# Kernel optimization log

Hardware: AMD Instinct MI355X
Metric: run time of the kernel (lower is better)

## Reference

```python
import jax, jax.numpy as jnp
import numpy as np

VX, VY = 0.16, 0.16
X0, Y0 = 0.0, -39.68
BN_EPS = 1e-5
P, M, C_IN, C_OUT = 40000, 100, 9, 64


def setup_inputs() -> dict:
    key = jax.random.key(0)
    ks = jax.random.split(key, 8)
    return {
        "pillar_x": jax.random.normal(ks[0], (P, M), dtype=jnp.float32),
        "pillar_y": jax.random.normal(ks[1], (P, M), dtype=jnp.float32),
        "pillar_z": jax.random.normal(ks[2], (P, M), dtype=jnp.float32),
        "pillar_i": jax.random.uniform(ks[3], (P, M), dtype=jnp.float32),
        "num_points_per_pillar": jax.random.randint(ks[4], (P,), 0, M, dtype=jnp.int32),
        "coors": jax.random.randint(ks[5], (P, 4), 0, 496, dtype=jnp.int32),
        "W": jax.random.normal(ks[6], (C_IN, C_OUT), dtype=jnp.float32) * 0.1,
        "gamma": jnp.ones((C_OUT,), dtype=jnp.float32),
        "beta": jnp.zeros((C_OUT,), dtype=jnp.float32),
    }


def reference(pillar_x, pillar_y, pillar_z, pillar_i, num_points_per_pillar, coors, W, gamma, beta):
    dtype = pillar_x.dtype
    max_points = pillar_x.shape[1]
    # per-pillar point count, clamped to >=1 (matches torch.clamp(min=1))
    n = jnp.clip(num_points_per_pillar, 1, None).astype(dtype)[:, None]  # (P,1)
    mean_x = jnp.sum(pillar_x, axis=1, keepdims=True) / n
    mean_y = jnp.sum(pillar_y, axis=1, keepdims=True) / n
    mean_z = jnp.sum(pillar_z, axis=1, keepdims=True) / n
    x_off = pillar_x - mean_x
    y_off = pillar_y - mean_y
    z_off = pillar_z - mean_z
    # BEV pillar-center coordinates, broadcast over points
    x_bev = (coors[:, 3].astype(dtype) * VX + VX / 2 + X0)[:, None] * jnp.ones((1, max_points), dtype)
    y_bev = (coors[:, 2].astype(dtype) * VY + VY / 2 + Y0)[:, None] * jnp.ones((1, max_points), dtype)
    # validity mask: point index < num_points (vectorized version of the python loop)
    mask = (jnp.arange(max_points)[None, :] < num_points_per_pillar[:, None]).astype(dtype)
    feats = jnp.stack(
        [pillar_x, pillar_y, pillar_z, pillar_i, x_off, y_off, z_off, x_bev, y_bev],
        axis=-1,
    )  # (P, M, 9)
    feats = feats * mask[:, :, None]
    # PFNLayer: Linear (no bias) -> BatchNorm1d (training-mode batch stats) -> ReLU -> max over points
    x = jnp.einsum("pmc,cd->pmd", feats, W)  # (P, M, 64)
    mu = jnp.mean(x, axis=(0, 1))
    var = jnp.var(x, axis=(0, 1))  # biased variance, as BatchNorm uses
    x = (x - mu) * jax.lax.rsqrt(var + BN_EPS) * gamma + beta
    x = jax.nn.relu(x)
    return jnp.max(x, axis=1)  # (P, 64)
```

## Files before the change

### kernel.cpp

```cpp
#include <hip/hip_runtime.h>

#define P_N 40000
#define M_N 100
#define NBF 10000
#define NPART 80
#define NUSED 74
#define NBUCKET 32

typedef _Float16 half2_t __attribute__((ext_vector_type(2)));

__device__ __forceinline__ float bcf(int x) { return __int_as_float(x); }
__device__ __forceinline__ int   bci(float x) { return __float_as_int(x); }
__device__ __forceinline__ float rlf(float v, int l) {
  return bcf(__builtin_amdgcn_readlane(bci(v), l));
}
__device__ __forceinline__ int pk16i(float a, float b) {
  return __builtin_bit_cast(int, __builtin_amdgcn_cvt_pkrtz(a, b));
}
__device__ __forceinline__ half2_t h2(int x) { return __builtin_bit_cast(half2_t, x); }
__device__ __forceinline__ float dot2(int a, int b, float acc) {
  return __builtin_amdgcn_fdot2(h2(a), h2(b), acc, false);
}

__device__ __forceinline__ float dpp_sum64(float x) {
  x += bcf(__builtin_amdgcn_update_dpp(0, bci(x), 0x111, 0xf, 0xf, true));
  x += bcf(__builtin_amdgcn_update_dpp(0, bci(x), 0x112, 0xf, 0xf, true));
  x += bcf(__builtin_amdgcn_update_dpp(0, bci(x), 0x114, 0xf, 0xf, true));
  x += bcf(__builtin_amdgcn_update_dpp(0, bci(x), 0x118, 0xf, 0xf, true));
  x += bcf(__builtin_amdgcn_update_dpp(0, bci(x), 0x142, 0xf, 0xf, true));
  x += bcf(__builtin_amdgcn_update_dpp(0, bci(x), 0x143, 0xf, 0xf, true));
  return x;
}

__device__ __forceinline__ half2_t uPK(int4 q, half2_t AA, half2_t BB,
                                       half2_t CC, half2_t DD, half2_t EE) {
  half2_t t = h2(q.w) * DD + EE;
  t = h2(q.z) * CC + t;
  t = h2(q.y) * BB + t;
  t = h2(q.x) * AA + t;
  return t;
}


__global__ __launch_bounds__(256) void k_zero(float* __restrict__ buckets) {
  const int i = threadIdx.x;
  #pragma unroll
  for (int k = 0; k < NBUCKET * NPART / 256; ++k) buckets[k * 256 + i] = 0.f;
}


__global__ __launch_bounds__(128) void k_fused(
    const float* __restrict__ px, const float* __restrict__ py,
    const float* __restrict__ pz, const float* __restrict__ pi,
    const int* __restrict__ npp, const int* __restrict__ coors,
    const float* __restrict__ W,
    float* __restrict__ buckets, float* __restrict__ umm)
{
  const int lane = threadIdx.x & 63;
  const int wid  = threadIdx.x >> 6;
  const int d    = lane;

  __shared__ int4  stage[2][2][64];
  __shared__ float red[2][NPART];

  int c = 9, c2 = 9;
  if (lane < 45) {
    int k = lane; c = 0;
    while (k >= 9 - c) { k -= 9 - c; ++c; }
    c2 = c + k;
  } else if (lane < 54) {
    c = lane - 45; c2 = 9;
  }
  const int rc1 = (c  < 4) ? c  : (c  < 7) ? c  - 4 : (c  < 9) ? c  - 2 : 4;
  const int rc2 = (c2 < 4) ? c2 : (c2 < 7) ? c2 - 4 : (c2 < 9) ? c2 - 2 : 4;
  const bool bothVec = (rc1 < 4) && (rc2 < 4);
  const bool statln  = lane < 54;

  float w[9];
  #pragma unroll
  for (int q = 0; q < 9; ++q) w[q] = W[q * 64 + d];
  const float sA = w[0] + w[4], sB = w[1] + w[5], sC = w[2] + w[6], sD = w[3];
  const half2_t AA = h2(pk16i(sA, sA));
  const half2_t BB = h2(pk16i(sB, sB));
  const half2_t CC = h2(pk16i(sC, sC));
  const half2_t DD = h2(pk16i(sD, sD));
  const int H1 = 0x3C003C00;

  const bool act = lane < 50;
  const int wgid  = blockIdx.x * 2 + wid;
  const int pbase = __builtin_amdgcn_readfirstlane(wgid * 2);

  const int2 n2 = ((const int2*)npp)[wgid];
  int4 cc[2];
  cc[0] = ((const int4*)coors)[pbase + 0];
  cc[1] = ((const int4*)coors)[pbase + 1];

  int u0[2], u1[2], u2[2], u3[2];
  #pragma unroll
  for (int it = 0; it < 2; ++it) {
    const int p_ = pbase + it;
    float2 X = make_float2(0.f, 0.f), Y = X, Z = X, I = X;
    if (act) {
      X = ((const float2*)(px + (size_t)p_ * M_N))[lane];
      Y = ((const float2*)(py + (size_t)p_ * M_N))[lane];
      Z = ((const float2*)(pz + (size_t)p_ * M_N))[lane];
      I = ((const float2*)(pi + (size_t)p_ * M_N))[lane];
    }
    u0[it] = pk16i(X.x, X.y);
    u1[it] = pk16i(Y.x, Y.y);
    u2[it] = pk16i(Z.x, Z.y);
    u3[it] = pk16i(I.x, I.y);
    stage[wid][it][lane] = make_int4(u0[it], u1[it], u2[it], u3[it]);
  }

  float R2a[10] = {};
  float corrAcc = 0.f;

  #pragma unroll
  for (int it = 0; it < 2; ++it) {
    const int p_ = pbase + it;
    const int n  = ((const int*)&n2)[it];
    const float nf = (float)n;

    const unsigned msk = ((2 * lane     < n) ? 0x0000FFFFu : 0u)
                       | ((2 * lane + 1 < n) ? 0xFFFF0000u : 0u);
    const int g0 = u0[it] & msk;
    const int g1 = u1[it] & msk;
    const int g2 = u2[it] & msk;
    const int g3 = u3[it] & msk;

    float fx = dot2(u0[it], H1, 0.f);
    float fy = dot2(u1[it], H1, 0.f);
    float fz = dot2(u2[it], H1, 0.f);
    float vx = dot2(g0, H1, 0.f);
    float vy = dot2(g1, H1, 0.f);
    float vz = dot2(g2, H1, 0.f);
    float vi = dot2(g3, H1, 0.f);
    fx = dpp_sum64(fx); fy = dpp_sum64(fy); fz = dpp_sum64(fz);
    vx = dpp_sum64(vx); vy = dpp_sum64(vy); vz = dpp_sum64(vz); vi = dpp_sum64(vi);

    const int nc = n < 1 ? 1 : n;
    const float inv = __builtin_amdgcn_rcpf((float)nc);
    const float mx = rlf(fx, 63) * inv;
    const float my = rlf(fy, 63) * inv;
    const float mz = rlf(fz, 63) * inv;
    const float svx = rlf(vx, 63);
    const float svy = rlf(vy, 63);
    const float svz = rlf(vz, 63);
    const float svi = rlf(vi, 63);

    const float xb = fmaf((float)cc[it].w, 0.16f, 0.08f);
    const float yb = fmaf((float)cc[it].z, 0.16f, 0.08f - 39.68f);

    R2a[0] = dot2(g0, g0, R2a[0]);
    R2a[1] = dot2(g0, g1, R2a[1]);
    R2a[2] = dot2(g0, g2, R2a[2]);
    R2a[3] = dot2(g0, g3, R2a[3]);
    R2a[4] = dot2(g1, g1, R2a[4]);
    R2a[5] = dot2(g1, g2, R2a[5]);
    R2a[6] = dot2(g1, g3, R2a[6]);
    R2a[7] = dot2(g2, g2, R2a[7]);
    R2a[8] = dot2(g2, g3, R2a[8]);
    R2a[9] = dot2(g3, g3, R2a[9]);

    {
      const float nxb = nf * xb, nyb = nf * yb;
      const float S1 = (rc1 == 0) ? svx : (rc1 == 1) ? svy : (rc1 == 2) ? svz
                     : (rc1 == 3) ? svi : (rc1 == 4) ? nf  : (rc1 == 5) ? nxb : nyb;
      const float S2 = (rc2 == 0) ? svx : (rc2 == 1) ? svy : (rc2 == 2) ? svz
                     : (rc2 == 3) ? svi : (rc2 == 4) ? nf  : (rc2 == 5) ? nxb : nyb;
      float base = 0.f;
      if (!bothVec)
        base = (rc1 > 3) ? ((rc1 == 4) ? S2 : (rc1 == 5) ? xb * S2 : yb * S2)
                         : ((rc2 == 4) ? S1 : (rc2 == 5) ? xb * S1 : yb * S1);
      const float mv1 = (c  == 4) ? mx : (c  == 5) ? my : (c  == 6) ? mz : 0.f;
      const float mv2 = (c2 == 4) ? mx : (c2 == 5) ? my : (c2 == 6) ? mz : 0.f;
      const float term = base - mv1 * S2 - mv2 * S1 + nf * mv1 * mv2;
      if (statln) corrAcc += term;
    }

    const float sE = fmaf(-mx, w[4], fmaf(-my, w[5], fmaf(-mz, w[6],
                     fmaf(xb, w[7], yb * w[8]))));
    const half2_t EE = h2(pk16i(sE, sE));

    const int4* sp = &stage[wid][it][0];
    half2_t ap0 = h2((int)0xFC00FC00);
    half2_t ap1 = ap0;
    const int nh = n >> 1;
    int l = 0;
    for (; l + 2 <= nh; l += 2) {
      const int4 qa = sp[l];
      const int4 qb = sp[l + 1];
      ap0 = __builtin_elementwise_max(ap0, uPK(qa, AA, BB, CC, DD, EE));
      ap1 = __builtin_elementwise_max(ap1, uPK(qb, AA, BB, CC, DD, EE));
    }
    if (l < nh)
      ap0 = __builtin_elementwise_max(ap0, uPK(sp[l], AA, BB, CC, DD, EE));
    const half2_t am = __builtin_elementwise_max(ap0, ap1);
    float um = fmaxf((float)am.x, (float)am.y);
    if (n & 1) {
      const int4 qt = sp[nh];
      const float tx = (float)h2(qt.x).x;
      const float ty = (float)h2(qt.y).x;
      const float tz = (float)h2(qt.z).x;
      const float ti = (float)h2(qt.w).x;
      um = fmaxf(um, fmaf(tx, sA, fmaf(ty, sB, fmaf(tz, sC, fmaf(ti, sD, sE)))));
    }
    umm[(size_t)p_ * 64 + d] = um;
  }

  #pragma unroll
  for (int i = 0; i < 10; ++i) R2a[i] = dpp_sum64(R2a[i]);

  red[wid][lane] = corrAcc;
  if (lane == 63) {
    #pragma unroll
    for (int i = 0; i < 10; ++i) red[wid][64 + i] = R2a[i];
  }
  __syncthreads();
  if (threadIdx.x < NUSED) {
    const int t = threadIdx.x;
    atomicAdd(&buckets[(blockIdx.x & (NBUCKET - 1)) * NPART + t],
              red[0][t] + red[1][t]);
  }
}


__global__ __launch_bounds__(64) void k_stats(
    const float* __restrict__ buckets, const float* __restrict__ W,
    const float* __restrict__ gamma, const float* __restrict__ beta,
    float* __restrict__ scale, float* __restrict__ shift)
{
  const int d = threadIdx.x;
  __shared__ float Cs[NUSED];
  {
    float s0 = 0.f, s1 = 0.f;
    #pragma unroll
    for (int b = 0; b < NBUCKET; ++b) {
      s0 += buckets[b * NPART + d];
      if (d < NUSED - 64) s1 += buckets[b * NPART + 64 + d];
    }
    Cs[d] = s0;
    if (d < NUSED - 64) Cs[64 + d] = s1;
  }
  __syncthreads();

  float mom1[9];
  #pragma unroll
  for (int q = 0; q < 9; ++q) mom1[q] = Cs[45 + q];
  float mom2[45];
  {
    int k = 0;
    #pragma unroll
    for (int cA = 0; cA < 9; ++cA) {
      #pragma unroll
      for (int cB = cA; cB < 9; ++cB) {
        float v = Cs[k];
        if (cA <= 6 && cB <= 6) {
          const int a = (cA < 4) ? cA : cA - 4;
          const int b = (cB < 4) ? cB : cB - 4;
          const int lo = a < b ? a : b;
          const int hi = a < b ? b : a;
          const int idx = lo * 4 - lo * (lo - 1) / 2 + (hi - lo);
          v += Cs[64 + idx];
        }
        mom2[k] = v;
        ++k;
      }
    }
  }

  float w[9];
  #pragma unroll
  for (int q = 0; q < 9; ++q) w[q] = W[q * 64 + d];
  const float invN = 1.f / ((float)P_N * (float)M_N);
  float mu = 0.f;
  #pragma unroll
  for (int q = 0; q < 9; ++q) mu += mom1[q] * w[q];
  mu *= invN;
  float e2 = 0.f;
  int k = 0;
  #pragma unroll
  for (int cA = 0; cA < 9; ++cA) {
    #pragma unroll
    for (int cB = cA; cB < 9; ++cB) {
      const float t = w[cA] * w[cB] * mom2[k];
      e2 += (cA == cB) ? t : 2.f * t;
      ++k;
    }
  }
  e2 *= invN;
  float var = e2 - mu * mu;
  var = var < 0.f ? 0.f : var;
  const float sc = gamma[d] * rsqrtf(var + 1e-5f);
  const float sh = fmaf(-mu, sc, beta[d]);
  scale[d] = sc;
  shift[d] = sh;
}


__global__ __launch_bounds__(256) void k_apply(
    const int* __restrict__ npp, const float* __restrict__ scale,
    const float* __restrict__ shift, float* __restrict__ out)
{
  const int gid = blockIdx.x * 256 + threadIdx.x;
  const int p = gid >> 4;
  const int q = gid & 15;

  float4 u4 = ((const float4*)out)[gid];
  const float4 sc4 = ((const float4*)scale)[q];
  const float4 sh4 = ((const float4*)shift)[q];
  const int n = npp[p];
  const bool has_masked = n < M_N;

  float4 r;
  float t;
  t = fmaf(sc4.x, u4.x, sh4.x); if (has_masked) t = fmaxf(t, sh4.x); r.x = fmaxf(t, 0.f);
  t = fmaf(sc4.y, u4.y, sh4.y); if (has_masked) t = fmaxf(t, sh4.y); r.y = fmaxf(t, 0.f);
  t = fmaf(sc4.z, u4.z, sh4.z); if (has_masked) t = fmaxf(t, sh4.z); r.z = fmaxf(t, 0.f);
  t = fmaf(sc4.w, u4.w, sh4.w); if (has_masked) t = fmaxf(t, sh4.w); r.w = fmaxf(t, 0.f);
  ((float4*)out)[gid] = r;
}


extern "C" void kernel_launch(void* const* d_in, const int* in_sizes, int n_in,
                              void* d_out, int out_size, void* d_ws, size_t ws_size,
                              hipStream_t stream) {
  const float* px    = (const float*)d_in[0];
  const float* py    = (const float*)d_in[1];
  const float* pz    = (const float*)d_in[2];
  const float* pi    = (const float*)d_in[3];
  const int*   npp   = (const int*)d_in[4];
  const int*   coors = (const int*)d_in[5];
  const float* W     = (const float*)d_in[6];
  const float* gamma = (const float*)d_in[7];
  const float* beta  = (const float*)d_in[8];
  float* out = (float*)d_out;

  float* wsf     = (float*)d_ws;
  float* buckets = wsf;
  float* scale   = wsf + 2560;
  float* shift   = wsf + 2624;

  k_zero<<<1, 256, 0, stream>>>(buckets);
  k_fused<<<NBF, 128, 0, stream>>>(px, py, pz, pi, npp, coors, W, buckets, out);
  k_stats<<<1, 64, 0, stream>>>(buckets, W, gamma, beta, scale, shift);
  k_apply<<<P_N * 64 / 4 / 256, 256, 0, stream>>>(npp, scale, shift, out);
}
```

Measured before the change: 58.38 us.

## Compute per-point projection with MFMA instead of packed-half FMA loop

Replaces the packed fp16 FMA loop over valid points with 32x32x16 fp16 MFMA instructions. Points are restaged as (x,y,z,i) half quads, with invalid points filled by NaN so that fmax drops them. The max over 128 point slots is taken via register and shuffle reductions, and the per-pillar offset sE is added afterwards. This removes the variable-length loop and its LDS-bound FMA work but always processes all point slots and wastes half the MFMA K dimension.

```diff
diff --git a/kernel.cpp b/kernel.cpp
--- a/kernel.cpp
+++ b/kernel.cpp
@@ -8,6 +8,8 @@
 #define NBUCKET 32
 
 typedef _Float16 half2_t __attribute__((ext_vector_type(2)));
+typedef _Float16 half8_t __attribute__((ext_vector_type(8)));
+typedef float    f32x16 __attribute__((ext_vector_type(16)));
 
 __device__ __forceinline__ float bcf(int x) { return __int_as_float(x); }
 __device__ __forceinline__ int   bci(float x) { return __float_as_int(x); }
@@ -18,6 +20,7 @@
   return __builtin_bit_cast(int, __builtin_amdgcn_cvt_pkrtz(a, b));
 }
 __device__ __forceinline__ half2_t h2(int x) { return __builtin_bit_cast(half2_t, x); }
+__device__ __forceinline__ half8_t h8(int4 v) { return __builtin_bit_cast(half8_t, v); }
 __device__ __forceinline__ float dot2(int a, int b, float acc) {
   return __builtin_amdgcn_fdot2(h2(a), h2(b), acc, false);
 }
@@ -30,15 +33,6 @@
   x += bcf(__builtin_amdgcn_update_dpp(0, bci(x), 0x142, 0xf, 0xf, true));
   x += bcf(__builtin_amdgcn_update_dpp(0, bci(x), 0x143, 0xf, 0xf, true));
   return x;
-}
-
-__device__ __forceinline__ half2_t uPK(int4 q, half2_t AA, half2_t BB,
-                                       half2_t CC, half2_t DD, half2_t EE) {
-  half2_t t = h2(q.w) * DD + EE;
-  t = h2(q.z) * CC + t;
-  t = h2(q.y) * BB + t;
-  t = h2(q.x) * AA + t;
-  return t;
 }
 
 
@@ -80,11 +74,20 @@
   #pragma unroll
   for (int q = 0; q < 9; ++q) w[q] = W[q * 64 + d];
   const float sA = w[0] + w[4], sB = w[1] + w[5], sC = w[2] + w[6], sD = w[3];
-  const half2_t AA = h2(pk16i(sA, sA));
-  const half2_t BB = h2(pk16i(sB, sB));
-  const half2_t CC = h2(pk16i(sC, sC));
-  const half2_t DD = h2(pk16i(sD, sD));
   const int H1 = 0x3C003C00;
+
+  const int pAB = pk16i(sA, sB);
+  const int pCD = pk16i(sC, sD);
+  const bool lo32 = lane < 32;
+  half8_t Bf[2];
+  #pragma unroll
+  for (int j = 0; j < 2; ++j) {
+    const int src = 32 * j + (lane & 31);
+    const int b0 = __shfl(pAB, src);
+    const int b1 = __shfl(pCD, src);
+    Bf[j] = h8(make_int4(lo32 ? b0 : 0, lo32 ? b1 : 0, 0, 0));
+  }
+  const f32x16 Z16 = (f32x16)0.0f;
 
   const bool act = lane < 50;
   const int wgid  = blockIdx.x * 2 + wid;
@@ -99,6 +102,7 @@
   #pragma unroll
   for (int it = 0; it < 2; ++it) {
     const int p_ = pbase + it;
+    const int n_ = ((const int*)&n2)[it];
     float2 X = make_float2(0.f, 0.f), Y = X, Z = X, I = X;
     if (act) {
       X = ((const float2*)(px + (size_t)p_ * M_N))[lane];
@@ -110,7 +114,15 @@
     u1[it] = pk16i(Y.x, Y.y);
     u2[it] = pk16i(Z.x, Z.y);
     u3[it] = pk16i(I.x, I.y);
-    stage[wid][it][lane] = make_int4(u0[it], u1[it], u2[it], u3[it]);
+    const int NN = 0x7E007E00;
+    const bool v0 = (2 * lane)     < n_;
+    const bool v1 = (2 * lane + 1) < n_;
+    int4 pm;
+    pm.x = v0 ? pk16i(X.x, Y.x) : NN;
+    pm.y = v0 ? pk16i(Z.x, I.x) : NN;
+    pm.z = v1 ? pk16i(X.y, Y.y) : NN;
+    pm.w = v1 ? pk16i(Z.y, I.y) : NN;
+    stage[wid][it][lane] = pm;
   }
 
   float R2a[10] = {};
@@ -181,31 +193,34 @@
 
     const float sE = fmaf(-mx, w[4], fmaf(-my, w[5], fmaf(-mz, w[6],
                      fmaf(xb, w[7], yb * w[8]))));
-    const half2_t EE = h2(pk16i(sE, sE));
-
-    const int4* sp = &stage[wid][it][0];
-    half2_t ap0 = h2((int)0xFC00FC00);
-    half2_t ap1 = ap0;
-    const int nh = n >> 1;
-    int l = 0;
-    for (; l + 2 <= nh; l += 2) {
-      const int4 qa = sp[l];
-      const int4 qb = sp[l + 1];
-      ap0 = __builtin_elementwise_max(ap0, uPK(qa, AA, BB, CC, DD, EE));
-      ap1 = __builtin_elementwise_max(ap1, uPK(qb, AA, BB, CC, DD, EE));
-    }
-    if (l < nh)
-      ap0 = __builtin_elementwise_max(ap0, uPK(sp[l], AA, BB, CC, DD, EE));
-    const half2_t am = __builtin_elementwise_max(ap0, ap1);
-    float um = fmaxf((float)am.x, (float)am.y);
-    if (n & 1) {
-      const int4 qt = sp[nh];
-      const float tx = (float)h2(qt.x).x;
-      const float ty = (float)h2(qt.y).x;
-      const float tz = (float)h2(qt.z).x;
-      const float ti = (float)h2(qt.w).x;
-      um = fmaxf(um, fmaf(tx, sA, fmaf(ty, sB, fmaf(tz, sC, fmaf(ti, sD, sE)))));
-    }
+
+    const int2* sp2 = (const int2*)&stage[wid][it][0];
+    f32x16 R0, R1;
+    #pragma unroll
+    for (int t = 0; t < 4; ++t) {
+      int2 pa = make_int2(0, 0);
+      if (lo32) pa = sp2[32 * t + (lane & 31)];
+      const half8_t A = h8(make_int4(pa.x, pa.y, 0, 0));
+      const f32x16 c0 = __builtin_amdgcn_mfma_f32_32x32x16_f16(A, Bf[0], Z16, 0, 0, 0);
+      const f32x16 c1 = __builtin_amdgcn_mfma_f32_32x32x16_f16(A, Bf[1], Z16, 0, 0, 0);
+      if (t == 0) { R0 = c0; R1 = c1; }
+      else {
+        R0 = __builtin_elementwise_max(R0, c0);
+        R1 = __builtin_elementwise_max(R1, c1);
+      }
+    }
+    #pragma unroll
+    for (int s = 8; s; s >>= 1) {
+      #pragma unroll
+      for (int i = 0; i < s; ++i) {
+        R0[i] = fmaxf(R0[i], R0[i + s]);
+        R1[i] = fmaxf(R1[i], R1[i + s]);
+      }
+    }
+    float m0 = R0[0], m1 = R1[0];
+    m0 = fmaxf(m0, __shfl_xor(m0, 32));
+    m1 = fmaxf(m1, __shfl_xor(m1, 32));
+    const float um = ((lane < 32) ? m0 : m1) + sE;
     umm[(size_t)p_ * 64 + d] = um;
   }
 
```

New measurement: 84.18 us. 44.2% more time.
